# Performance work log

Measured on AMD Instinct MI355X. Metric: run time of the kernel, lower is better.

Reference implementation:

```python
import jax, jax.numpy as jnp
import numpy as np

ANISO = (0.096, 0.096, 0.096)
BIG = 1e10  # stands in for +inf feature distance
SMOOTH = 1e-05


def _minplus(f, axis, w):
    # exact 1D squared distance transform along `axis` via min-plus conv:
    # g[i] = min_j f[j] + (w*(i-j))^2 ; vectorized over all other dims.
    f = jnp.moveaxis(f, axis, -1)
    n = f.shape[-1]
    idx = jnp.arange(n, dtype=f.dtype)
    d2 = (w * (idx[:, None] - idx[None, :])) ** 2  # [j, i]
    g = jnp.min(f[..., :, None] + d2, axis=-2)
    return jnp.moveaxis(g, -1, axis)


def _edt_multilabel(labels, num_labels):
    # labels: [b, X, Y, Z] int, values in [1, num_labels]
    # Multi-label euclidean distance transform (edt.edt semantics on gt+1):
    # for each voxel, distance to nearest voxel carrying a DIFFERENT label,
    # scaled by ANISO. Computed as per-label squared EDT fields (separable
    # min-plus per axis, exact) combined by excluding the voxel's own label.
    fields = []
    for L in range(1, num_labels + 1):  # small fixed loop over classes
        f = jnp.where(labels == L, 0.0, BIG).astype(jnp.float32)
        for ax, w in zip((1, 2, 3), ANISO):
            f = _minplus(f, ax, w)
        fields.append(f)
    D = jnp.stack(fields, axis=0)  # [L, b, X, Y, Z] squared distances
    own = jnp.moveaxis(jax.nn.one_hot(labels - 1, num_labels, dtype=jnp.float32), -1, 0)
    d2 = jnp.min(jnp.where(own > 0, BIG, D), axis=0)  # nearest different label
    return jnp.sqrt(d2)


def setup_inputs() -> dict:
    key = jax.random.key(0)
    kx, ky = jax.random.split(key)
    x = jax.random.uniform(kx, (2, 3, 64, 64, 64), dtype=jnp.float32)  # softmax probs
    y = jax.random.randint(ky, (2, 1, 64, 64, 64), 0, 3)  # label map, classes 0..2
    return {"x": x, "y": y}


def reference(x, y):
    b, c = x.shape[:2]
    yi = y[:, 0]  # [b, X, Y, Z]
    # scatter_(1, gt, 1) -> one hot over channel dim
    y_onehot = jnp.moveaxis(jax.nn.one_hot(yi, c, dtype=x.dtype), -1, 1)  # [b,c,X,Y,Z]
    # dt = edt(gt + 1) + 1 ; all labels >=1 so every voxel is 'foreground'
    dt = (_edt_multilabel(yi + 1, c) + 1.0)[:, None]  # [b,1,X,Y,Z]
    fp = x * (1.0 - y_onehot) * dt
    fn = (1.0 - x) * y_onehot * dt
    # do_bg=False (non-batch-dice path): drop background channel
    fp = fp[:, 1:]
    fn = fn[:, 1:]
    return jnp.mean(fp) + jnp.mean(fn) + SMOOTH
```

## Files before the change

### kernel.cpp

```cpp
#include <hip/hip_runtime.h>
#include <math.h>

#define BIGV 10000000000.0f
#define WA   0.096f
#define ABSENT 16000

typedef short short2v __attribute__((ext_vector_type(2)));

__device__ __forceinline__ short2v pack2(int a, int b) {
    short2v r; r.x = (short)a; r.y = (short)b; return r;
}

__device__ __forceinline__ short seed_d2_i16(unsigned long long mask, int i) {
    const unsigned long long mr = mask >> i;
    const unsigned long long ml = mask << (63 - i);
    const int dr = mr ? __builtin_ctzll(mr) : 127;
    const int dl = ml ? __builtin_clzll(ml) : 127;
    const int d  = dr < dl ? dr : dl;
    return (short)(d > 63 ? ABSENT : d * d);
}

__global__ __launch_bounds__(256) void pass_xz_kernel(const int* __restrict__ lab,
                                                      unsigned short* __restrict__ D,
                                                      float* __restrict__ out) {
    if (blockIdx.x == 0 && blockIdx.y == 0 && blockIdx.z == 0 && threadIdx.x == 0)
        out[0] = 1e-5f;

    const int ys = blockIdx.x, b = blockIdx.y, zq = blockIdx.z;
    const int lane = threadIdx.x & 63;
    const int wv   = threadIdx.x >> 6;

    __shared__ short sm[3][64][64];

    const int* lp = lab + b * 262144 + ys * 64;
    for (int z = wv * 16, e = z + 16; z < e; ++z) {
        const int lv = lp[z * 4096 + lane];
        sm[0][z][lane] = seed_d2_i16(__ballot(lv == 0), lane);
        sm[1][z][lane] = seed_d2_i16(__ballot(lv == 1), lane);
        sm[2][z][lane] = seed_d2_i16(__ballot(lv == 2), lane);
    }
    __syncthreads();

    const int i0 = zq * 16 + wv * 4;
    short2v mA0 = {32767, 32767}, mA1 = mA0;
    short2v mB0 = mA0, mB1 = mA0, mC0 = mA0, mC1 = mA0;

    for (int j = 0; j < 64; ++j) {
        const short a0 = sm[0][j][lane];
        const short a1 = sm[1][j][lane];
        const short a2 = sm[2][j][lane];
        const short2v a0p = {a0, a0}, a1p = {a1, a1}, a2p = {a2, a2};
        const int dz = i0 - j;
        const short2v d2p0 = pack2(dz * dz, (dz + 1) * (dz + 1));
        const short2v d2p1 = pack2((dz + 2) * (dz + 2), (dz + 3) * (dz + 3));
        mA0 = __builtin_elementwise_min(mA0, (short2v)(a0p + d2p0));
        mA1 = __builtin_elementwise_min(mA1, (short2v)(a0p + d2p1));
        mB0 = __builtin_elementwise_min(mB0, (short2v)(a1p + d2p0));
        mB1 = __builtin_elementwise_min(mB1, (short2v)(a1p + d2p1));
        mC0 = __builtin_elementwise_min(mC0, (short2v)(a2p + d2p0));
        mC1 = __builtin_elementwise_min(mC1, (short2v)(a2p + d2p1));
    }

    unsigned short* Dp = D + b * 3 * 262144 + ys * 64 + lane;
    const int r0 = i0 * 4096;
    Dp[r0]                       = (unsigned short)mA0.x;
    Dp[r0 + 4096]                = (unsigned short)mA0.y;
    Dp[r0 + 2 * 4096]            = (unsigned short)mA1.x;
    Dp[r0 + 3 * 4096]            = (unsigned short)mA1.y;
    Dp[262144 + r0]              = (unsigned short)mB0.x;
    Dp[262144 + r0 + 4096]       = (unsigned short)mB0.y;
    Dp[262144 + r0 + 2 * 4096]   = (unsigned short)mB1.x;
    Dp[262144 + r0 + 3 * 4096]   = (unsigned short)mB1.y;
    Dp[524288 + r0]              = (unsigned short)mC0.x;
    Dp[524288 + r0 + 4096]       = (unsigned short)mC0.y;
    Dp[524288 + r0 + 2 * 4096]   = (unsigned short)mC1.x;
    Dp[524288 + r0 + 3 * 4096]   = (unsigned short)mC1.y;
}

__global__ __launch_bounds__(256) void pass_y_kernel(const float* __restrict__ x,
                                                     const int* __restrict__ lab,
                                                     const unsigned short* __restrict__ D,
                                                     float* __restrict__ out) {
    const int z = blockIdx.x, b = blockIdx.y, yq = blockIdx.z;
    const int lane = threadIdx.x & 63;
    const int wv   = threadIdx.x >> 6;

    __shared__ short sm[3][64][64];
    {
        const uint4* Dp4 = (const uint4*)(D + b * 3 * 262144 + z * 4096);
        uint4* s4 = (uint4*)&sm[0][0][0];
        for (int t = threadIdx.x; t < 512; t += 256) {
            s4[t]        = Dp4[t];
            s4[512 + t]  = Dp4[32768 + t];
            s4[1024 + t] = Dp4[65536 + t];
        }
    }

    const int i0 = yq * 16 + wv * 4;
    int   lv[4];
    float x1[4], x2[4];
#pragma unroll
    for (int ii = 0; ii < 4; ++ii) {
        const int off = z * 4096 + (i0 + ii) * 64 + lane;
        lv[ii] = lab[b * 262144 + off];
        x1[ii] = x[(b * 3 + 1) * 262144 + off];
        x2[ii] = x[(b * 3 + 2) * 262144 + off];
    }
    __syncthreads();

    short2v mA0 = {32767, 32767}, mA1 = mA0;
    short2v mB0 = mA0, mB1 = mA0, mC0 = mA0, mC1 = mA0;

    for (int j = 0; j < 64; ++j) {
        const short a0 = sm[0][j][lane];
        const short a1 = sm[1][j][lane];
        const short a2 = sm[2][j][lane];
        const short2v a0p = {a0, a0}, a1p = {a1, a1}, a2p = {a2, a2};
        const int dy = i0 - j;
        const short2v d2p0 = pack2(dy * dy, (dy + 1) * (dy + 1));
        const short2v d2p1 = pack2((dy + 2) * (dy + 2), (dy + 3) * (dy + 3));
        mA0 = __builtin_elementwise_min(mA0, (short2v)(a0p + d2p0));
        mA1 = __builtin_elementwise_min(mA1, (short2v)(a0p + d2p1));
        mB0 = __builtin_elementwise_min(mB0, (short2v)(a1p + d2p0));
        mB1 = __builtin_elementwise_min(mB1, (short2v)(a1p + d2p1));
        mC0 = __builtin_elementwise_min(mC0, (short2v)(a2p + d2p0));
        mC1 = __builtin_elementwise_min(mC1, (short2v)(a2p + d2p1));
    }

    const int g0[4] = {mA0.x, mA0.y, mA1.x, mA1.y};
    const int g1[4] = {mB0.x, mB0.y, mB1.x, mB1.y};
    const int g2[4] = {mC0.x, mC0.y, mC1.x, mC1.y};

    float part = 0.0f;
#pragma unroll
    for (int ii = 0; ii < 4; ++ii) {
        const int e0 = (lv[ii] == 0) ? (1 << 20) : g0[ii];
        const int e1 = (lv[ii] == 1) ? (1 << 20) : g1[ii];
        const int e2 = (lv[ii] == 2) ? (1 << 20) : g2[ii];
        const int dm = min(e0, min(e1, e2));
        const float d2f = (dm >= ABSENT) ? BIGV : (float)dm * (WA * WA);
        const float dt  = sqrtf(d2f) + 1.0f;
        const float t1  = (lv[ii] == 1) ? (1.0f - x1[ii]) : x1[ii];
        const float t2  = (lv[ii] == 2) ? (1.0f - x2[ii]) : x2[ii];
        part += (t1 + t2) * dt;
    }

#pragma unroll
    for (int o = 32; o; o >>= 1) part += __shfl_down(part, o);
    if (lane == 0)
        atomicAdd(out, part * (1.0f / 1048576.0f));
}

extern "C" void kernel_launch(void* const* d_in, const int* in_sizes, int n_in,
                              void* d_out, int out_size, void* d_ws, size_t ws_size,
                              hipStream_t stream) {
    const float* x = (const float*)d_in[0];
    const int*   y = (const int*)d_in[1];
    unsigned short* D = (unsigned short*)d_ws;
    float* out = (float*)d_out;

    pass_xz_kernel<<<dim3(64, 2, 4), 256, 0, stream>>>(y, D, out);
    pass_y_kernel<<<dim3(64, 2, 4), 256, 0, stream>>>(x, y, D, out);
}
```

Baseline: 98.26 us.

## Transpose LDS tiles with XOR swizzle so each lane reads 16-byte vectors

Shared memory is reorganised so each lane's 64-entry column is contiguous, with an XOR swizzle on the 8-element chunk index. The min-plus scan can then load eight values per LDS instruction instead of one scalar short per step, and it is factored into a shared scan64 helper. The squared-distance offsets are carried forward from earlier iterations rather than recomputed. In exchange, the pass_y staging now scatters individual shorts into the transposed layout, which adds many narrow LDS stores and possible bank conflicts during the load phase.

Result: no change. 97.21 us (-1.1%).

```diff
diff --git a/kernel.cpp b/kernel.cpp
--- a/kernel.cpp
+++ b/kernel.cpp
@@ -6,6 +6,7 @@
 #define ABSENT 16000
 
 typedef short short2v __attribute__((ext_vector_type(2)));
+typedef short short8v __attribute__((ext_vector_type(8)));
 
 __device__ __forceinline__ short2v pack2(int a, int b) {
     short2v r; r.x = (short)a; r.y = (short)b; return r;
@@ -20,6 +21,45 @@
     return (short)(d > 63 ? ABSENT : d * d);
 }
 
+struct Acc { short2v A0, A1, B0, B1, C0, C1; };
+
+__device__ __forceinline__ Acc scan64(const short* __restrict__ smb,
+                                      int lane, int i0) {
+    Acc m;
+    m.A0 = (short2v){32767, 32767};
+    m.A1 = m.A0; m.B0 = m.A0; m.B1 = m.A0; m.C0 = m.A0; m.C1 = m.A0;
+
+    const int xr = lane & 7;
+    short2v d2m2 = pack2((i0 + 2) * (i0 + 2), (i0 + 3) * (i0 + 3));
+    short2v d2m1 = pack2((i0 + 1) * (i0 + 1), (i0 + 2) * (i0 + 2));
+
+#pragma unroll
+    for (int c = 0; c < 8; ++c) {
+        const int base = lane * 64 + ((c ^ xr) << 3);
+        const short8v a0 = *(const short8v*)(smb + base);
+        const short8v a1 = *(const short8v*)(smb + 4096 + base);
+        const short8v a2 = *(const short8v*)(smb + 8192 + base);
+#pragma unroll
+        for (int k = 0; k < 8; ++k) {
+            const int j  = c * 8 + k;
+            const int dz = i0 - j;
+            const short2v cur = pack2(dz * dz, (dz + 1) * (dz + 1));
+            const short2v dP  = d2m2;
+            const short2v a0p = {a0[k], a0[k]};
+            const short2v a1p = {a1[k], a1[k]};
+            const short2v a2p = {a2[k], a2[k]};
+            m.A0 = __builtin_elementwise_min(m.A0, (short2v)(a0p + cur));
+            m.A1 = __builtin_elementwise_min(m.A1, (short2v)(a0p + dP));
+            m.B0 = __builtin_elementwise_min(m.B0, (short2v)(a1p + cur));
+            m.B1 = __builtin_elementwise_min(m.B1, (short2v)(a1p + dP));
+            m.C0 = __builtin_elementwise_min(m.C0, (short2v)(a2p + cur));
+            m.C1 = __builtin_elementwise_min(m.C1, (short2v)(a2p + dP));
+            d2m2 = d2m1; d2m1 = cur;
+        }
+    }
+    return m;
+}
+
 __global__ __launch_bounds__(256) void pass_xz_kernel(const int* __restrict__ lab,
                                                       unsigned short* __restrict__ D,
                                                       float* __restrict__ out) {
@@ -29,52 +69,48 @@
     const int ys = blockIdx.x, b = blockIdx.y, zq = blockIdx.z;
     const int lane = threadIdx.x & 63;
     const int wv   = threadIdx.x >> 6;
+    const int xr   = lane & 7;
 
     __shared__ short sm[3][64][64];
+    short* smb = &sm[0][0][0];
 
     const int* lp = lab + b * 262144 + ys * 64;
-    for (int z = wv * 16, e = z + 16; z < e; ++z) {
-        const int lv = lp[z * 4096 + lane];
-        sm[0][z][lane] = seed_d2_i16(__ballot(lv == 0), lane);
-        sm[1][z][lane] = seed_d2_i16(__ballot(lv == 1), lane);
-        sm[2][z][lane] = seed_d2_i16(__ballot(lv == 2), lane);
+#pragma unroll
+    for (int zz = 0; zz < 2; ++zz) {
+        const int zb = 2 * wv + zz;
+        short8v s0, s1, s2;
+#pragma unroll
+        for (int k = 0; k < 8; ++k) {
+            const int z  = zb * 8 + k;
+            const int lv = lp[z * 4096 + lane];
+            s0[k] = seed_d2_i16(__ballot(lv == 0), lane);
+            s1[k] = seed_d2_i16(__ballot(lv == 1), lane);
+            s2[k] = seed_d2_i16(__ballot(lv == 2), lane);
+        }
+        const int base = lane * 64 + ((zb ^ xr) << 3);
+        *(short8v*)(smb + base)        = s0;
+        *(short8v*)(smb + 4096 + base) = s1;
+        *(short8v*)(smb + 8192 + base) = s2;
     }
     __syncthreads();
 
     const int i0 = zq * 16 + wv * 4;
-    short2v mA0 = {32767, 32767}, mA1 = mA0;
-    short2v mB0 = mA0, mB1 = mA0, mC0 = mA0, mC1 = mA0;
-
-    for (int j = 0; j < 64; ++j) {
-        const short a0 = sm[0][j][lane];
-        const short a1 = sm[1][j][lane];
-        const short a2 = sm[2][j][lane];
-        const short2v a0p = {a0, a0}, a1p = {a1, a1}, a2p = {a2, a2};
-        const int dz = i0 - j;
-        const short2v d2p0 = pack2(dz * dz, (dz + 1) * (dz + 1));
-        const short2v d2p1 = pack2((dz + 2) * (dz + 2), (dz + 3) * (dz + 3));
-        mA0 = __builtin_elementwise_min(mA0, (short2v)(a0p + d2p0));
-        mA1 = __builtin_elementwise_min(mA1, (short2v)(a0p + d2p1));
-        mB0 = __builtin_elementwise_min(mB0, (short2v)(a1p + d2p0));
-        mB1 = __builtin_elementwise_min(mB1, (short2v)(a1p + d2p1));
-        mC0 = __builtin_elementwise_min(mC0, (short2v)(a2p + d2p0));
-        mC1 = __builtin_elementwise_min(mC1, (short2v)(a2p + d2p1));
-    }
+    const Acc m = scan64(smb, lane, i0);
 
     unsigned short* Dp = D + b * 3 * 262144 + ys * 64 + lane;
     const int r0 = i0 * 4096;
-    Dp[r0]                       = (unsigned short)mA0.x;
-    Dp[r0 + 4096]                = (unsigned short)mA0.y;
-    Dp[r0 + 2 * 4096]            = (unsigned short)mA1.x;
-    Dp[r0 + 3 * 4096]            = (unsigned short)mA1.y;
-    Dp[262144 + r0]              = (unsigned short)mB0.x;
-    Dp[262144 + r0 + 4096]       = (unsigned short)mB0.y;
-    Dp[262144 + r0 + 2 * 4096]   = (unsigned short)mB1.x;
-    Dp[262144 + r0 + 3 * 4096]   = (unsigned short)mB1.y;
-    Dp[524288 + r0]              = (unsigned short)mC0.x;
-    Dp[524288 + r0 + 4096]       = (unsigned short)mC0.y;
-    Dp[524288 + r0 + 2 * 4096]   = (unsigned short)mC1.x;
-    Dp[524288 + r0 + 3 * 4096]   = (unsigned short)mC1.y;
+    Dp[r0]                       = (unsigned short)m.A0.x;
+    Dp[r0 + 4096]                = (unsigned short)m.A0.y;
+    Dp[r0 + 2 * 4096]            = (unsigned short)m.A1.x;
+    Dp[r0 + 3 * 4096]            = (unsigned short)m.A1.y;
+    Dp[262144 + r0]              = (unsigned short)m.B0.x;
+    Dp[262144 + r0 + 4096]       = (unsigned short)m.B0.y;
+    Dp[262144 + r0 + 2 * 4096]   = (unsigned short)m.B1.x;
+    Dp[262144 + r0 + 3 * 4096]   = (unsigned short)m.B1.y;
+    Dp[524288 + r0]              = (unsigned short)m.C0.x;
+    Dp[524288 + r0 + 4096]       = (unsigned short)m.C0.y;
+    Dp[524288 + r0 + 2 * 4096]   = (unsigned short)m.C1.x;
+    Dp[524288 + r0 + 3 * 4096]   = (unsigned short)m.C1.y;
 }
 
 __global__ __launch_bounds__(256) void pass_y_kernel(const float* __restrict__ x,
@@ -86,13 +122,27 @@
     const int wv   = threadIdx.x >> 6;
 
     __shared__ short sm[3][64][64];
+    short* smb = &sm[0][0][0];
+
     {
-        const uint4* Dp4 = (const uint4*)(D + b * 3 * 262144 + z * 4096);
-        uint4* s4 = (uint4*)&sm[0][0][0];
-        for (int t = threadIdx.x; t < 512; t += 256) {
-            s4[t]        = Dp4[t];
-            s4[512 + t]  = Dp4[32768 + t];
-            s4[1024 + t] = Dp4[65536 + t];
+        const unsigned short* Dp = D + b * 3 * 262144 + z * 4096;
+#pragma unroll
+        for (int tt = 0; tt < 2; ++tt) {
+            const int t  = (int)threadIdx.x + tt * 256;
+            const int y  = t >> 3;
+            const int x0 = (t & 7) << 3;
+            const int yc = (y >> 3);
+            const int yl = (y & 7);
+#pragma unroll
+            for (int L = 0; L < 3; ++L) {
+                const uint4 v = ((const uint4*)(Dp + L * 262144))[t];
+                const unsigned int ww[4] = {v.x, v.y, v.z, v.w};
+#pragma unroll
+                for (int k = 0; k < 8; ++k) {
+                    const short e = (short)(ww[k >> 1] >> ((k & 1) << 4));
+                    smb[L * 4096 + (x0 + k) * 64 + ((yc ^ k) << 3) + yl] = e;
+                }
+            }
         }
     }
 
@@ -108,28 +158,11 @@
     }
     __syncthreads();
 
-    short2v mA0 = {32767, 32767}, mA1 = mA0;
-    short2v mB0 = mA0, mB1 = mA0, mC0 = mA0, mC1 = mA0;
+    const Acc m = scan64(smb, lane, i0);
 
-    for (int j = 0; j < 64; ++j) {
-        const short a0 = sm[0][j][lane];
-        const short a1 = sm[1][j][lane];
-        const short a2 = sm[2][j][lane];
-        const short2v a0p = {a0, a0}, a1p = {a1, a1}, a2p = {a2, a2};
-        const int dy = i0 - j;
-        const short2v d2p0 = pack2(dy * dy, (dy + 1) * (dy + 1));
-        const short2v d2p1 = pack2((dy + 2) * (dy + 2), (dy + 3) * (dy + 3));
-        mA0 = __builtin_elementwise_min(mA0, (short2v)(a0p + d2p0));
-        mA1 = __builtin_elementwise_min(mA1, (short2v)(a0p + d2p1));
-        mB0 = __builtin_elementwise_min(mB0, (short2v)(a1p + d2p0));
-        mB1 = __builtin_elementwise_min(mB1, (short2v)(a1p + d2p1));
-        mC0 = __builtin_elementwise_min(mC0, (short2v)(a2p + d2p0));
-        mC1 = __builtin_elementwise_min(mC1, (short2v)(a2p + d2p1));
-    }
-
-    const int g0[4] = {mA0.x, mA0.y, mA1.x, mA1.y};
-    const int g1[4] = {mB0.x, mB0.y, mB1.x, mB1.y};
-    const int g2[4] = {mC0.x, mC0.y, mC1.x, mC1.y};
+    const int g0[4] = {m.A0.x, m.A0.y, m.A1.x, m.A1.y};
+    const int g1[4] = {m.B0.x, m.B0.y, m.B1.x, m.B1.y};
+    const int g2[4] = {m.C0.x, m.C0.y, m.C1.x, m.C1.y};
 
     float part = 0.0f;
 #pragma unroll
```
